# Optimization experiments

Hardware: AMD Instinct MI355X
Metric: run time of the kernel (lower is better)

The kernel has to match this reference:

```python
import jax, jax.numpy as jnp
from jax import lax
import numpy as np

BLOCKS = 6
DIM = 768
D_STATE = 16
D_CONV = 4
EXPAND = 2
HEADDIM = 64
D_INNER = EXPAND * DIM              # 1536
NHEADS = D_INNER // HEADDIM        # 24
CONV_DIM = D_INNER + 2 * D_STATE   # 1568 (ngroups=1)
D_IN_PROJ = 2 * D_INNER + 2 * D_STATE + NHEADS  # 3128
NPITCH = 128


def setup_inputs() -> dict:
    key = jax.random.key(0)
    ks = jax.random.split(key, 16)
    B, L = 4, 4096
    s = 0.02
    return {
        "x": jax.random.normal(ks[0], (B, L, DIM), jnp.float32),
        "type_IDs": jax.random.randint(ks[1], (B, L), 0, 2),
        "in_proj_w": jax.random.normal(ks[2], (BLOCKS, D_IN_PROJ, DIM), jnp.float32) * s,
        "conv_w": jax.random.normal(ks[3], (BLOCKS, CONV_DIM, D_CONV), jnp.float32) * 0.1,
        "conv_b": jnp.zeros((BLOCKS, CONV_DIM), jnp.float32),
        "dt_bias": jax.random.uniform(ks[4], (BLOCKS, NHEADS), jnp.float32, -4.0, -2.0),
        "A_log": jnp.tile(jnp.log(jnp.linspace(1.0, 16.0, NHEADS, dtype=jnp.float32)), (BLOCKS, 1)),
        "D": jnp.ones((BLOCKS, NHEADS), jnp.float32),
        "norm_w": jnp.ones((BLOCKS, D_INNER), jnp.float32),
        "out_proj_w": jax.random.normal(ks[5], (BLOCKS, DIM, D_INNER), jnp.float32) * s,
        "head_w": jax.random.normal(ks[6], (2, DIM, DIM), jnp.float32) * s,
        "head_b": jnp.zeros((2, DIM), jnp.float32),
        "head_out_w": jax.random.normal(ks[7], (2, 4, NPITCH, DIM), jnp.float32) * s,
        "head_out_b": jnp.zeros((2, 4, NPITCH), jnp.float32),
    }


def _mamba2_block(x, Wi, cw, cb, dtb, Alog, Dp, nw, Wo):
    B, L, _ = x.shape
    zxbcdt = jnp.einsum('bld,ed->ble', x, Wi)                 # [B,L,D_IN_PROJ]
    z = zxbcdt[..., :D_INNER]
    xBC = zxbcdt[..., D_INNER:D_INNER + CONV_DIM]
    dt = zxbcdt[..., -NHEADS:]
    # causal depthwise conv1d over time
    xc = jnp.pad(jnp.swapaxes(xBC, 1, 2), ((0, 0), (0, 0), (D_CONV - 1, 0)))
    xBC = lax.conv_general_dilated(xc, cw[:, None, :], (1,), 'VALID',
                                   feature_group_count=CONV_DIM,
                                   dimension_numbers=('NCH', 'OIH', 'NCH'))
    xBC = jax.nn.silu(jnp.swapaxes(xBC, 1, 2) + cb)            # [B,L,CONV_DIM]
    xs = xBC[..., :D_INNER].reshape(B, L, NHEADS, HEADDIM)
    Bm = xBC[..., D_INNER:D_INNER + D_STATE]                   # [B,L,N]
    Cm = xBC[..., D_INNER + D_STATE:]                          # [B,L,N]
    dt = jax.nn.softplus(dt + dtb)                             # [B,L,H]
    dA = jnp.exp(dt * (-jnp.exp(Alog)))                        # [B,L,H]
    dtx = dt[..., None] * xs                                   # [B,L,H,P]

    def step(h, inp):
        dA_t, dtx_t, B_t, C_t = inp
        h = h * dA_t[:, :, None, None] + dtx_t[..., None] * B_t[:, None, None, :]
        y = jnp.einsum('bhpn,bn->bhp', h, C_t)
        return h, y

    h0 = jnp.zeros((B, NHEADS, HEADDIM, D_STATE), x.dtype)
    mv = lambda a: jnp.moveaxis(a, 1, 0)
    _, ys = lax.scan(step, h0, (mv(dA), mv(dtx), mv(Bm), mv(Cm)))
    y = jnp.moveaxis(ys, 0, 1) + Dp[None, None, :, None] * xs   # [B,L,H,P]
    y = y.reshape(B, L, D_INNER) * jax.nn.silu(z)               # gated
    y = y * lax.rsqrt(jnp.mean(y * y, -1, keepdims=True) + 1e-5) * nw
    return jnp.einsum('bli,di->bld', y, Wo)


def _head(t, hw, hb, ow, ob):
    h = jnp.einsum('bld,ed->ble', t, hw) + hb
    velocity = jnp.einsum('bld,pd->blp', h, ow[0]) + ob[0]
    onset = jax.nn.sigmoid(jnp.einsum('bld,pd->blp', h, ow[1]) + ob[1])
    offset = jax.nn.sigmoid(jnp.einsum('bld,pd->blp', h, ow[2]) + ob[2])
    frames = jax.nn.sigmoid(jnp.einsum('bld,pd->blp', h, ow[3]) + ob[3])
    return velocity, frames, onset, offset


def reference(x, type_IDs, in_proj_w, conv_w, conv_b, dt_bias, A_log, D,
              norm_w, out_proj_w, head_w, head_b, head_out_w, head_out_b):
    for i in range(BLOCKS):
        x = _mamba2_block(x, in_proj_w[i], conv_w[i], conv_b[i], dt_bias[i],
                          A_log[i], D[i], norm_w[i], out_proj_w[i])
    cmask = (type_IDs == 0).astype(x.dtype)[..., None]
    fmask = (type_IDs == 1).astype(x.dtype)[..., None]
    cv, cf, con, coff = _head(x, head_w[0], head_b[0], head_out_w[0], head_out_b[0])
    fv, ff, fon, foff = _head(x, head_w[1], head_b[1], head_out_w[1], head_out_b[1])
    # masked (instead of ragged boolean gather) to stay jit-compatible
    return jnp.stack([cv * cmask, cf * cmask, con * cmask, coff * cmask,
                      fv * fmask, ff * fmask, fon * fmask, foff * fmask])
```

## Files before the change

### kernel.cpp

```cpp
#include <hip/hip_runtime.h>
#include <cstdint>
#include <cstddef>

#define L_SEQ   4096
#define BATCH   4
#define DIMM    768
#define D_INNER 1536
#define NHEADS  24
#define HEADDIM 64
#define D_STATE 16
#define CONVD   1568
#define D_IPROJ 3128
#define ZXP     3200
#define SEGLEN  64
#define NSEG    (L_SEQ / SEGLEN)
#define BCP     44

typedef _Float16 f16x8 __attribute__((ext_vector_type(8)));
typedef _Float16 f16x4 __attribute__((ext_vector_type(4)));
typedef float    f32x4 __attribute__((ext_vector_type(4)));

__device__ __forceinline__ void glds16(const _Float16* g, _Float16* l) {
  __builtin_amdgcn_global_load_lds(
      (__attribute__((address_space(1))) unsigned int*)g,
      (__attribute__((address_space(3))) unsigned int*)l, 16, 0, 0);
}

__device__ __forceinline__ float fsilu(float x) {
  return x * __builtin_amdgcn_rcpf(1.f + __expf(-x));
}
__device__ __forceinline__ float fsig(float x) {
  return __builtin_amdgcn_rcpf(1.f + __expf(-x));
}

template <int OM>
__global__ __launch_bounds__(256, 2) void gemm_mfma(
    const _Float16* __restrict__ A, int lda,
    const _Float16* __restrict__ W,
    const float* __restrict__ bias,
    void* __restrict__ Cv, long ldc, long extra,
    int M, int N, int K,
    const int* __restrict__ tidsp, int thead)
{
  __shared__ __align__(16) char smem[33792];
  _Float16* As = (_Float16*)smem;
  _Float16* Ws = (_Float16*)(smem + 16384);
  const int tid = threadIdx.x;
  const int lane = tid & 63, wid = tid >> 6;
  const int wr = wid >> 1, wc = wid & 1;

  const int nbx = gridDim.x, nby = gridDim.y;
  const int flat = blockIdx.y * nbx + blockIdx.x;
  const int xcd = flat & 7;
  const int bidx = flat >> 3;
  const int rpx = nby >> 3;
  const int rl = bidx % rpx;
  const int ct = bidx / rpx;
  const long m0 = (long)(xcd * rpx + rl) * 128;
  const int n0 = ct * 128;

  const int la = lane & 15, lg = lane >> 4;
  const int srow = lane >> 3, schunk = lane & 7;

  f32x4 acc[4][4] = {};

  for (int k0 = 0; k0 < K; k0 += 64) {
    __syncthreads();
#pragma unroll
    for (int p = 0; p < 4; ++p) {
      const int rg = (wid << 2) + p;
      const int row = (rg << 3) + srow;
      const int scn = schunk ^ (row & 7);
      glds16(A + (m0 + row) * (long)lda + k0 + scn * 8, As + rg * 512);
      int n = n0 + row; if (n >= N) n = N - 1;
      glds16(W + (long)n * K + k0 + scn * 8, Ws + rg * 512);
    }
    asm volatile("s_waitcnt vmcnt(0)" ::: "memory");
    __syncthreads();
#pragma unroll
    for (int ks = 0; ks < 2; ++ks) {
      const int cc = ks * 4 + lg;
      f16x8 af[4], bfr[4];
#pragma unroll
      for (int i = 0; i < 4; ++i) {
        int ra = wr * 64 + i * 16 + la;
        int rb = wc * 64 + i * 16 + la;
        af[i]  = *(const f16x8*)&As[ra * 64 + ((cc ^ (ra & 7)) << 3)];
        bfr[i] = *(const f16x8*)&Ws[rb * 64 + ((cc ^ (rb & 7)) << 3)];
      }
#pragma unroll
      for (int i = 0; i < 4; ++i)
#pragma unroll
        for (int j = 0; j < 4; ++j)
          acc[i][j] = __builtin_amdgcn_mfma_f32_16x16x32_f16(af[i], bfr[j], acc[i][j], 0, 0, 0);
    }
  }

  float* epi = (float*)smem;
#pragma unroll
  for (int ph = 0; ph < 2; ++ph) {
    __syncthreads();
    if (wr == ph) {
#pragma unroll
      for (int i = 0; i < 4; ++i)
#pragma unroll
        for (int j = 0; j < 4; ++j)
#pragma unroll
          for (int r = 0; r < 4; ++r)
            epi[(i * 16 + lg * 4 + r) * 132 + wc * 64 + j * 16 + la] = acc[i][j][r];
    }
    __syncthreads();
    if (OM == 3) {
      const int q = n0 >> 7;
      const int rr = tid >> 5;
      const int ch = tid & 31;
#pragma unroll
      for (int ps = 0; ps < 8; ++ps) {
        int lrow = ps * 8 + rr;
        long gr = m0 + ph * 64 + lrow;
        float keep = (tidsp[gr] == thead) ? 1.f : 0.f;
        float4 v = *(float4*)&epi[lrow * 132 + ch * 4];
        float o[4] = {v.x, v.y, v.z, v.w};
#pragma unroll
        for (int e = 0; e < 4; ++e) {
          float vv = o[e] + bias[n0 + ch * 4 + e];
          if (q != 0) vv = fsig(vv);
          o[e] = vv * keep;
        }
        *(float4*)((float*)Cv + (long)q * extra + gr * 128 + ch * 4) =
            make_float4(o[0], o[1], o[2], o[3]);
      }
    } else {
      const int rr = tid >> 4;
      const int ch = tid & 15;
      const int col = n0 + ch * 8;
      float b[8] = {0.f, 0.f, 0.f, 0.f, 0.f, 0.f, 0.f, 0.f};
      if (OM == 2 && col < N) {
#pragma unroll
        for (int e = 0; e < 8; ++e) b[e] = bias[col + e];
      }
#pragma unroll
      for (int ps = 0; ps < 4; ++ps) {
        int lrow = ps * 16 + rr;
        long gr = m0 + ph * 64 + lrow;
        if (col < N) {
          float4 v0 = *(float4*)&epi[lrow * 132 + ch * 8];
          float4 v1 = *(float4*)&epi[lrow * 132 + ch * 8 + 4];
          f16x8 o = {(_Float16)(v0.x + b[0]), (_Float16)(v0.y + b[1]),
                     (_Float16)(v0.z + b[2]), (_Float16)(v0.w + b[3]),
                     (_Float16)(v1.x + b[4]), (_Float16)(v1.y + b[5]),
                     (_Float16)(v1.z + b[6]), (_Float16)(v1.w + b[7])};
          *(f16x8*)((_Float16*)Cv + gr * ldc + col) = o;
        }
      }
    }
  }
}

__global__ __launch_bounds__(256) void cvt_kernel(
    const float* __restrict__ src, _Float16* __restrict__ dst, long n4)
{
  long i = (long)blockIdx.x * 256 + threadIdx.x;
  long stride = (long)gridDim.x * 256;
  for (; i < n4; i += stride) {
    float4 v = *(const float4*)(src + i * 4);
    f16x4 o = { (_Float16)v.x, (_Float16)v.y, (_Float16)v.z, (_Float16)v.w };
    *(f16x4*)(dst + i * 4) = o;
  }
}

__global__ __launch_bounds__(256) void pack_head_kernel(
    const float* __restrict__ how, const float* __restrict__ hob,
    _Float16* __restrict__ howb, float* __restrict__ hobp)
{
  const int wmap[4] = {0, 3, 1, 2};
  int idx = blockIdx.x * 256 + threadIdx.x;
  if (idx < 2 * 512 * 768) {
    int t = idx / (512 * 768);
    int rem = idx - t * 512 * 768;
    int q = rem / (128 * 768);
    int rem2 = rem - q * 128 * 768;
    howb[idx] = (_Float16)how[((size_t)(t * 4 + wmap[q])) * 128 * 768 + rem2];
  }
  if (idx < 1024) {
    int t = idx >> 9, rem = idx & 511;
    int q = rem >> 7, pp = rem & 127;
    hobp[idx] = hob[(t * 4 + wmap[q]) * 128 + pp];
  }
}

__global__ __launch_bounds__(64) void ssdA_kernel(
    const _Float16* __restrict__ zx, const float* __restrict__ cw,
    const float* __restrict__ cb, const float* __restrict__ dtb,
    const float* __restrict__ alog, const float* __restrict__ Dv,
    _Float16* __restrict__ ybuf, _Float16* __restrict__ bcbuf,
    float* __restrict__ Hseg, float* __restrict__ cumq)
{
  __shared__ __align__(16) char sm[14848];
  _Float16* XV    = (_Float16*)sm;
  _Float16* bcraw = (_Float16*)sm;
  _Float16* BC    = (_Float16*)(sm + 8448);
  float* sa  = (float*)(sm + 14080);
  float* sdt = (float*)(sm + 14336);
  float* sws = (float*)(sm + 14592);
  const int lane = threadIdx.x;
  const int seg = blockIdx.x & (NSEG - 1);
  const int bh = blockIdx.x >> 6;
  const int h = bh % NHEADS, b = bh / NHEADS;
  const int bl0 = b * L_SEQ + seg * SEGLEN;
  const float LOG2E = 1.44269504088896f;

  for (int i = lane; i < 67 * 4; i += 64) {
    int r = i >> 2, q = (i & 3) << 3;
    f16x8 v = {};
    if (seg > 0 || r >= 3)
      v = *(const f16x8*)&zx[(size_t)(bl0 - 3 + r) * ZXP + 2 * D_INNER + q];
    *(f16x8*)&bcraw[r * 32 + q] = v;
  }
  {
    float raw = (float)zx[(size_t)(bl0 + lane) * ZXP + (D_INNER + CONVD) + h] + dtb[h];
    float sp = (raw > 20.f) ? raw : log1pf(__expf(raw));
    sdt[lane] = sp;
    float av = __expf(alog[h]) * sp * LOG2E;
#pragma unroll
    for (int off = 1; off < 64; off <<= 1) {
      float tv = __shfl_up(av, off, 64);
      if (lane >= off) av += tv;
    }
    sa[lane] = av;
    cumq[(size_t)bh * L_SEQ + seg * SEGLEN + lane] = exp2f(-av);
    float alast = __shfl(av, 63, 64);
    sws[lane] = exp2f(av - alast) * sp;
  }
  __syncthreads();

  for (int i = lane; i < SEGLEN * 32; i += 64) {
    int t = i >> 5, c = i & 31;
    float acc = cb[D_INNER + c];
#pragma unroll
    for (int k = 0; k < 4; ++k)
      acc = fmaf(cw[(D_INNER + c) * 4 + k], (float)bcraw[(t + k) * 32 + c], acc);
    _Float16 sh = (_Float16)fsilu(acc);
    BC[t * BCP + c] = sh;
    bcbuf[(size_t)(bl0 + t) * 32 + c] = sh;
  }
  __syncthreads();

  const int xch = h * HEADDIM + lane;
  const _Float16* xg = zx + (size_t)bl0 * ZXP + D_INNER + xch;
  const float cwx0 = cw[xch * 4 + 0], cwx1 = cw[xch * 4 + 1];
  const float cwx2 = cw[xch * 4 + 2], cwx3 = cw[xch * 4 + 3];
  const float cbx = cb[xch];
  float xw0 = 0.f, xw1 = 0.f, xw2 = 0.f;
  if (seg > 0) {
    xw0 = (float)xg[-3 * (long)ZXP];
    xw1 = (float)xg[-2 * (long)ZXP];
    xw2 = (float)xg[-1 * (long)ZXP];
  }
  float xcur = (float)xg[0];
  for (int t = 0; t < SEGLEN; ++t) {
    float xnext = (t < SEGLEN - 1) ? (float)xg[(size_t)(t + 1) * ZXP] : 0.f;
    float xa = cbx;
    xa = fmaf(cwx0, xw0, xa);
    xa = fmaf(cwx1, xw1, xa);
    xa = fmaf(cwx2, xw2, xa);
    xa = fmaf(cwx3, xcur, xa);
    XV[t * 66 + lane] = (_Float16)fsilu(xa);
    xw0 = xw1; xw1 = xw2; xw2 = xcur; xcur = xnext;
  }
  __syncthreads();

  const int la = lane & 15, lg = lane >> 4;

  f16x4 Mfrag[4][4];
  {
    f16x4 cf[4];
    float sat[4];
#pragma unroll
    for (int tt = 0; tt < 4; ++tt) {
      cf[tt] = *(const f16x4*)&BC[(tt * 16 + la) * BCP + 16 + lg * 4];
      sat[tt] = sa[tt * 16 + la];
    }
#pragma unroll
    for (int st = 0; st < 4; ++st) {
      f16x4 bfA = *(const f16x4*)&BC[(st * 16 + la) * BCP + lg * 4];
#pragma unroll
      for (int tt = 0; tt < 4; ++tt) {
        f32x4 a1 = {};
        a1 = __builtin_amdgcn_mfma_f32_16x16x16f16(bfA, cf[tt], a1, 0, 0, 0);
        f16x4 m;
#pragma unroll
        for (int r = 0; r < 4; ++r) {
          int s = st * 16 + lg * 4 + r;
          int t = tt * 16 + la;
          float mv = 0.f;
          if (s <= t) mv = a1[r] * exp2f(sa[s] - sat[tt]);
          m[r] = (_Float16)mv;
        }
        Mfrag[st][tt] = m;
      }
    }
  }

  f16x4 b3[4];
#pragma unroll
  for (int st = 0; st < 4; ++st) {
    f16x4 v;
#pragma unroll
    for (int e = 0; e < 4; ++e)
      v[e] = BC[(st * 16 + lg * 4 + e) * BCP + la];
    b3[st] = v;
  }

  const float Dh = Dv[h];
  float* Hst = Hseg + ((size_t)bh * NSEG + seg) * 1024;
#pragma unroll
  for (int pt = 0; pt < 4; ++pt) {
    f16x4 bf[4], af3[4];
#pragma unroll
    for (int st = 0; st < 4; ++st) {
      f16x4 v, w;
#pragma unroll
      for (int e = 0; e < 4; ++e) {
        int s = st * 16 + lg * 4 + e;
        float xv = (float)XV[s * 66 + pt * 16 + la];
        v[e] = (_Float16)(xv * sdt[s]);
        w[e] = (_Float16)(xv * sws[s]);
      }
      bf[st] = v; af3[st] = w;
    }
#pragma unroll
    for (int tt = 0; tt < 4; ++tt) {
      f32x4 a2 = {};
#pragma unroll
      for (int st = 0; st < 4; ++st)
        a2 = __builtin_amdgcn_mfma_f32_16x16x16f16(Mfrag[st][tt], bf[st], a2, 0, 0, 0);
#pragma unroll
      for (int r = 0; r < 4; ++r) {
        int t = tt * 16 + lg * 4 + r, p = pt * 16 + la;
        float y = a2[r] + Dh * (float)XV[t * 66 + p];
        ybuf[(size_t)(bl0 + t) * D_INNER + h * HEADDIM + p] = (_Float16)y;
      }
    }
    f32x4 a3 = {};
#pragma unroll
    for (int st = 0; st < 4; ++st)
      a3 = __builtin_amdgcn_mfma_f32_16x16x16f16(af3[st], b3[st], a3, 0, 0, 0);
#pragma unroll
    for (int r = 0; r < 4; ++r) {
      int p = pt * 16 + lg * 4 + r;
      Hst[p * 16 + la] = a3[r];
    }
  }
}

__global__ __launch_bounds__(1024) void scanB_kernel(
    float* __restrict__ Hseg, const float* __restrict__ cumq)
{
  const int bh = blockIdx.x;
  const int t = threadIdx.x;
  __shared__ float sp[NSEG];
  if (t < NSEG) sp[t] = cumq[(size_t)bh * L_SEQ + t * SEGLEN + (SEGLEN - 1)];
  __syncthreads();
  float v[NSEG];
#pragma unroll
  for (int s = 0; s < NSEG; ++s)
    v[s] = Hseg[((size_t)bh * NSEG + s) * 1024 + t];
  float h = 0.f;
#pragma unroll
  for (int s = 0; s < NSEG; ++s) {
    Hseg[((size_t)bh * NSEG + s) * 1024 + t] = h;
    h = fmaf(sp[s], h, v[s]);
  }
}

__global__ __launch_bounds__(64) void ssdC_kernel(
    _Float16* __restrict__ ybuf, const _Float16* __restrict__ bcbuf,
    const float* __restrict__ Hseg, const float* __restrict__ cumq)
{
  const int seg = blockIdx.x & (NSEG - 1);
  if (seg == 0) return;
  const int lane = threadIdx.x;
  const int bh = blockIdx.x >> 6;
  const int h = bh % NHEADS, b = bh / NHEADS;
  const int bl0 = b * L_SEQ + seg * SEGLEN;
  __shared__ float scq[SEGLEN];
  scq[lane] = cumq[(size_t)bh * L_SEQ + seg * SEGLEN + lane];
  const int la = lane & 15, lg = lane >> 4;
  const float* slot = Hseg + ((size_t)bh * NSEG + seg) * 1024;

  f16x8 a4[4], w4[4];
#pragma unroll
  for (int i = 0; i < 4; ++i) {
    f16x8 v = {};
    if (lg < 2)
      v = *(const f16x8*)&bcbuf[(size_t)(bl0 + i * 16 + la) * 32 + 16 + lg * 8];
    a4[i] = v;
  }
#pragma unroll
  for (int j = 0; j < 4; ++j) {
    f16x8 v = {};
    if (lg < 2) {
#pragma unroll
      for (int e = 0; e < 8; ++e)
        v[e] = (_Float16)slot[(j * 16 + la) * 16 + lg * 8 + e];
    }
    w4[j] = v;
  }
  f32x4 acc[4][4] = {};
#pragma unroll
  for (int i = 0; i < 4; ++i)
#pragma unroll
    for (int j = 0; j < 4; ++j)
      acc[i][j] = __builtin_amdgcn_mfma_f32_16x16x32_f16(a4[i], w4[j], acc[i][j], 0, 0, 0);
  __syncthreads();
#pragma unroll
  for (int i = 0; i < 4; ++i)
#pragma unroll
    for (int j = 0; j < 4; ++j)
#pragma unroll
      for (int r = 0; r < 4; ++r) {
        int t = i * 16 + lg * 4 + r, p = j * 16 + la;
        size_t ad = (size_t)(bl0 + t) * D_INNER + h * HEADDIM + p;
        ybuf[ad] = (_Float16)((float)ybuf[ad] + scq[t] * acc[i][j][r]);
      }
}

__global__ __launch_bounds__(256) void norm_kernel(
    const _Float16* __restrict__ y, _Float16* __restrict__ zx,
    const float* __restrict__ nw)
{
  const int row = blockIdx.x;
  const int tid = threadIdx.x;
  const _Float16* yr = y + (size_t)row * D_INNER;
  _Float16* zr = zx + (size_t)row * ZXP;
  float v[6];
  float ss = 0.f;
#pragma unroll
  for (int jj = 0; jj < 6; ++jj) {
    int c = jj * 256 + tid;
    float yv = (float)yr[c];
    float zv = (float)zr[c];
    float val = yv * fsilu(zv);
    v[jj] = val;
    ss = fmaf(val, val, ss);
  }
#pragma unroll
  for (int off = 32; off > 0; off >>= 1) ss += __shfl_xor(ss, off, 64);
  __shared__ float red[4];
  if ((tid & 63) == 0) red[tid >> 6] = ss;
  __syncthreads();
  float tot = red[0] + red[1] + red[2] + red[3];
  float rs = rsqrtf(tot * (1.f / 1536.f) + 1e-5f);
#pragma unroll
  for (int jj = 0; jj < 6; ++jj) {
    int c = jj * 256 + tid;
    zr[c] = (_Float16)(v[jj] * rs * nw[c]);
  }
}

extern "C" void kernel_launch(void* const* d_in, const int* in_sizes, int n_in,
                              void* d_out, int out_size, void* d_ws, size_t ws_size,
                              hipStream_t stream)
{
  const float* x_in = (const float*)d_in[0];
  const int*   tids = (const int*)d_in[1];
  const float* ipw  = (const float*)d_in[2];
  const float* cw   = (const float*)d_in[3];
  const float* cb   = (const float*)d_in[4];
  const float* dtb  = (const float*)d_in[5];
  const float* alog = (const float*)d_in[6];
  const float* Dv   = (const float*)d_in[7];
  const float* nw   = (const float*)d_in[8];
  const float* opw  = (const float*)d_in[9];
  const float* hw   = (const float*)d_in[10];
  const float* hb   = (const float*)d_in[11];
  const float* how  = (const float*)d_in[12];
  const float* hob  = (const float*)d_in[13];
  float* out = (float*)d_out;

  char* p = (char*)d_ws;
  _Float16* ipw_b = (_Float16*)p; p += (size_t)14413824 * 2;
  _Float16* opw_b = (_Float16*)p; p += (size_t)7077888 * 2;
  _Float16* hw_b  = (_Float16*)p; p += (size_t)1179648 * 2;
  _Float16* how_b = (_Float16*)p; p += (size_t)786432 * 2;
  float*    hob_p = (float*)p;    p += (size_t)1024 * 4;
  const size_t used_w = (size_t)(p - (char*)d_ws);
  const size_t PB = 54528000;
  int nb = 4;
  while (nb > 1 && used_w + (size_t)nb * PB > ws_size) nb >>= 1;

  cvt_kernel<<<8192, 256, 0, stream>>>(ipw, ipw_b, 14413824 / 4);
  cvt_kernel<<<6912, 256, 0, stream>>>(opw, opw_b, 7077888 / 4);
  cvt_kernel<<<1152, 256, 0, stream>>>(hw, hw_b, 1179648 / 4);
  pack_head_kernel<<<3072, 256, 0, stream>>>(how, hob, how_b, hob_p);

  for (int b0 = 0; b0 < BATCH; b0 += nb) {
    const int MT = nb * L_SEQ;
    _Float16* zx    = (_Float16*)p;
    _Float16* ybuf  = zx + (size_t)MT * ZXP;
    _Float16* bcbuf = ybuf + (size_t)MT * D_INNER;
    float*    Hseg  = (float*)(bcbuf + (size_t)MT * 32);
    float*    cumq  = Hseg + (size_t)nb * NHEADS * NSEG * 1024;
    _Float16* xbuf  = (_Float16*)(cumq + (size_t)MT * NHEADS);
    _Float16* hbuf  = zx;

    cvt_kernel<<<6144, 256, 0, stream>>>(x_in + (size_t)b0 * L_SEQ * DIMM,
                                         xbuf, (long)MT * DIMM / 4);

    for (int i = 0; i < 6; ++i) {
      gemm_mfma<0><<<dim3((D_IPROJ + 127) / 128, MT / 128), 256, 0, stream>>>(
          xbuf, DIMM, ipw_b + (size_t)i * D_IPROJ * DIMM, nullptr,
          zx, ZXP, 0, MT, D_IPROJ, DIMM, nullptr, 0);
      ssdA_kernel<<<nb * NHEADS * NSEG, 64, 0, stream>>>(
          zx, cw + (size_t)i * CONVD * 4, cb + i * CONVD,
          dtb + i * NHEADS, alog + i * NHEADS, Dv + i * NHEADS,
          ybuf, bcbuf, Hseg, cumq);
      scanB_kernel<<<nb * NHEADS, 1024, 0, stream>>>(Hseg, cumq);
      ssdC_kernel<<<nb * NHEADS * NSEG, 64, 0, stream>>>(ybuf, bcbuf, Hseg, cumq);
      norm_kernel<<<MT, 256, 0, stream>>>(ybuf, zx, nw + i * D_INNER);
      gemm_mfma<0><<<dim3(DIMM / 128, MT / 128), 256, 0, stream>>>(
          zx, ZXP, opw_b + (size_t)i * DIMM * D_INNER, nullptr,
          xbuf, DIMM, 0, MT, DIMM, D_INNER, nullptr, 0);
    }

    for (int t = 0; t < 2; ++t) {
      gemm_mfma<2><<<dim3(DIMM / 128, MT / 128), 256, 0, stream>>>(
          xbuf, DIMM, hw_b + (size_t)t * DIMM * DIMM, hb + t * DIMM,
          hbuf, DIMM, 0, MT, DIMM, DIMM, nullptr, 0);
      gemm_mfma<3><<<dim3(4, MT / 128), 256, 0, stream>>>(
          hbuf, DIMM, how_b + (size_t)t * 512 * DIMM, hob_p + t * 512,
          out + (size_t)t * 4 * 16384 * 128 + (size_t)b0 * L_SEQ * 128,
          128, (long)16384 * 128, MT, 512, DIMM,
          tids + (size_t)b0 * L_SEQ, t);
    }
  }
}
```

Measured before the change: 1.785 ms.

## Add 256x256-tile 512-thread MFMA GEMM with double-buffered LDS for projections

Introduces a new GEMM kernel using 256x256 output tiles, 8 waves, a 64-wide K step with double-buffered direct global-to-LDS loads, XOR-swizzled LDS layout and an XCD-aware block mapping. The in-projection, out-projection and head hidden GEMMs now use it instead of the 128x128 kernel. The f16-output epilogue of the old kernel is removed because only its sigmoid/mask output path is still used. The larger tile raises arithmetic intensity and reuse per loaded byte, at the cost of one block per CU (128 KB LDS, heavy register use) and fewer blocks in flight, which could hurt tail balance on small N such as 768.

```diff
diff --git a/kernel.cpp b/kernel.cpp
--- a/kernel.cpp
+++ b/kernel.cpp
@@ -34,6 +34,127 @@
 }
 
 template <int OM>
+__global__ __launch_bounds__(512, 1) void gemm256(
+    const _Float16* __restrict__ A, long lda,
+    const _Float16* __restrict__ W,
+    const float* __restrict__ bias,
+    _Float16* __restrict__ C, long ldc,
+    int M, int N, int K)
+{
+  __shared__ __align__(16) _Float16 lds[65536];
+  const int tid = threadIdx.x;
+  const int lane = tid & 63, wid = tid >> 6;
+  const int wm = wid >> 2, wn = wid & 3;
+  const int la = lane & 15, lg = lane >> 4;
+  const int srow = lane >> 3, schunk = lane & 7;
+
+  const int nbx = gridDim.x, nby = gridDim.y;
+  const int flat = blockIdx.y * nbx + blockIdx.x;
+  const int xcd = flat & 7, idx = flat >> 3;
+  const int rpx = nby >> 3;
+  const long m0 = (long)(xcd * rpx + idx % rpx) * 256;
+  const int n0 = (idx / rpx) * 256;
+
+  const int nkt = K >> 6;
+
+  auto stage = [&](int buf, int ht, int kt) {
+#pragma unroll
+    for (int p = 0; p < 2; ++p) {
+      int rg = wid * 2 + p;
+      int rl = (ht & 1) * 128 + rg * 8 + srow;
+      int scn = schunk ^ (rl & 7);
+      const _Float16* src;
+      if (ht < 2) {
+        src = A + (m0 + rl) * lda + kt * 64 + scn * 8;
+      } else {
+        int n = n0 + rl; if (n >= N) n = N - 1;
+        src = W + (long)n * (long)K + kt * 64 + scn * 8;
+      }
+      _Float16* dst = lds + (ht >= 2 ? 32768 : 0) + buf * 16384
+                          + ((ht & 1) * 128 + rg * 8) * 64;
+      glds16(src, dst);
+    }
+  };
+
+  f32x4 acc[8][4] = {};
+
+  stage(0, 0, 0); stage(0, 1, 0); stage(0, 2, 0); stage(0, 3, 0);
+  asm volatile("s_waitcnt vmcnt(0)" ::: "memory");
+  __syncthreads();
+
+  int buf = 0;
+  for (int kt = 0; kt < nkt; ++kt) {
+    const bool nl = (kt + 1 < nkt);
+    const _Float16* Ab = lds + buf * 16384;
+    const _Float16* Bb = lds + 32768 + buf * 16384;
+    f16x8 bfr[4][2];
+#pragma unroll
+    for (int ph = 0; ph < 4; ++ph) {
+      if (nl) stage(buf ^ 1, ph, kt + 1);
+      if (ph == 0) {
+#pragma unroll
+        for (int j = 0; j < 4; ++j)
+#pragma unroll
+          for (int ks = 0; ks < 2; ++ks) {
+            int rb = wn * 64 + j * 16 + la;
+            int cc = ks * 4 + lg;
+            bfr[j][ks] = *(const f16x8*)&Bb[rb * 64 + ((cc ^ (rb & 7)) << 3)];
+          }
+      }
+      f16x8 af[2][2];
+#pragma unroll
+      for (int ii = 0; ii < 2; ++ii)
+#pragma unroll
+        for (int ks = 0; ks < 2; ++ks) {
+          int ra = wm * 128 + (ph * 2 + ii) * 16 + la;
+          int cc = ks * 4 + lg;
+          af[ii][ks] = *(const f16x8*)&Ab[ra * 64 + ((cc ^ (ra & 7)) << 3)];
+        }
+      __builtin_amdgcn_s_setprio(1);
+#pragma unroll
+      for (int ii = 0; ii < 2; ++ii)
+#pragma unroll
+        for (int j = 0; j < 4; ++j)
+#pragma unroll
+          for (int ks = 0; ks < 2; ++ks)
+            acc[ph * 2 + ii][j] = __builtin_amdgcn_mfma_f32_16x16x32_f16(
+                af[ii][ks], bfr[j][ks], acc[ph * 2 + ii][j], 0, 0, 0);
+      __builtin_amdgcn_s_setprio(0);
+      if (ph == 3 && nl) asm volatile("s_waitcnt vmcnt(0)" ::: "memory");
+      __syncthreads();
+    }
+    buf ^= 1;
+  }
+
+  _Float16* ep = lds + wid * 8192;
+#pragma unroll
+  for (int i = 0; i < 8; ++i)
+#pragma unroll
+    for (int j = 0; j < 4; ++j) {
+      float bs = 0.f;
+      if (OM == 2) bs = bias[n0 + wn * 64 + j * 16 + la];
+#pragma unroll
+      for (int r = 0; r < 4; ++r) {
+        int row = i * 16 + lg * 4 + r;
+        int jj = j ^ (row & 3);
+        ep[row * 64 + jj * 16 + la] = (_Float16)(acc[i][j][r] + bs);
+      }
+    }
+  asm volatile("s_waitcnt lgkmcnt(0)" ::: "memory");
+#pragma unroll
+  for (int it = 0; it < 16; ++it) {
+    int row = it * 8 + (lane >> 3);
+    int hc = lane & 7;
+    int jj = (hc >> 1) ^ (row & 3);
+    f16x8 v = *(const f16x8*)&ep[row * 64 + jj * 16 + (hc & 1) * 8];
+    int gcol = n0 + wn * 64 + hc * 8;
+    long grow = m0 + wm * 128 + row;
+    if (gcol < N)
+      *(f16x8*)&C[grow * ldc + gcol] = v;
+  }
+}
+
+template <int OM>
 __global__ __launch_bounds__(256, 2) void gemm_mfma(
     const _Float16* __restrict__ A, int lda,
     const _Float16* __restrict__ W,
@@ -129,29 +250,6 @@
         }
         *(float4*)((float*)Cv + (long)q * extra + gr * 128 + ch * 4) =
             make_float4(o[0], o[1], o[2], o[3]);
-      }
-    } else {
-      const int rr = tid >> 4;
-      const int ch = tid & 15;
-      const int col = n0 + ch * 8;
-      float b[8] = {0.f, 0.f, 0.f, 0.f, 0.f, 0.f, 0.f, 0.f};
-      if (OM == 2 && col < N) {
-#pragma unroll
-        for (int e = 0; e < 8; ++e) b[e] = bias[col + e];
-      }
-#pragma unroll
-      for (int ps = 0; ps < 4; ++ps) {
-        int lrow = ps * 16 + rr;
-        long gr = m0 + ph * 64 + lrow;
-        if (col < N) {
-          float4 v0 = *(float4*)&epi[lrow * 132 + ch * 8];
-          float4 v1 = *(float4*)&epi[lrow * 132 + ch * 8 + 4];
-          f16x8 o = {(_Float16)(v0.x + b[0]), (_Float16)(v0.y + b[1]),
-                     (_Float16)(v0.z + b[2]), (_Float16)(v0.w + b[3]),
-                     (_Float16)(v1.x + b[4]), (_Float16)(v1.y + b[5]),
-                     (_Float16)(v1.z + b[6]), (_Float16)(v1.w + b[7])};
-          *(f16x8*)((_Float16*)Cv + gr * ldc + col) = o;
-        }
       }
     }
   }
@@ -509,9 +607,9 @@
                                          xbuf, (long)MT * DIMM / 4);
 
     for (int i = 0; i < 6; ++i) {
-      gemm_mfma<0><<<dim3((D_IPROJ + 127) / 128, MT / 128), 256, 0, stream>>>(
+      gemm256<0><<<dim3(13, MT / 256), 512, 0, stream>>>(
           xbuf, DIMM, ipw_b + (size_t)i * D_IPROJ * DIMM, nullptr,
-          zx, ZXP, 0, MT, D_IPROJ, DIMM, nullptr, 0);
+          zx, ZXP, MT, D_IPROJ, DIMM);
       ssdA_kernel<<<nb * NHEADS * NSEG, 64, 0, stream>>>(
           zx, cw + (size_t)i * CONVD * 4, cb + i * CONVD,
           dtb + i * NHEADS, alog + i * NHEADS, Dv + i * NHEADS,
@@ -519,15 +617,15 @@
       scanB_kernel<<<nb * NHEADS, 1024, 0, stream>>>(Hseg, cumq);
       ssdC_kernel<<<nb * NHEADS * NSEG, 64, 0, stream>>>(ybuf, bcbuf, Hseg, cumq);
       norm_kernel<<<MT, 256, 0, stream>>>(ybuf, zx, nw + i * D_INNER);
-      gemm_mfma<0><<<dim3(DIMM / 128, MT / 128), 256, 0, stream>>>(
+      gemm256<0><<<dim3(3, MT / 256), 512, 0, stream>>>(
           zx, ZXP, opw_b + (size_t)i * DIMM * D_INNER, nullptr,
-          xbuf, DIMM, 0, MT, DIMM, D_INNER, nullptr, 0);
+          xbuf, DIMM, MT, DIMM, D_INNER);
     }
 
     for (int t = 0; t < 2; ++t) {
-      gemm_mfma<2><<<dim3(DIMM / 128, MT / 128), 256, 0, stream>>>(
+      gemm256<2><<<dim3(3, MT / 256), 512, 0, stream>>>(
           xbuf, DIMM, hw_b + (size_t)t * DIMM * DIMM, hb + t * DIMM,
-          hbuf, DIMM, 0, MT, DIMM, DIMM, nullptr, 0);
+          hbuf, DIMM, MT, DIMM, DIMM);
       gemm_mfma<3><<<dim3(4, MT / 128), 256, 0, stream>>>(
           hbuf, DIMM, how_b + (size_t)t * 512 * DIMM, hob_p + t * 512,
           out + (size_t)t * 4 * 16384 * 128 + (size_t)b0 * L_SEQ * 128,
```

After: 2.041 ms. 14.4% more time.
